# Kernel tuning notes

Hardware: AMD Instinct MI355X
Metric: run time of the kernel (lower is better)

## Reference

```python
import jax, jax.numpy as jnp
import numpy as np

N0 = N1 = N2 = N3 = 8          # input_shape
R = 8                           # input_ranks (rank_i)
L = 8                           # link_ranks (ring bond dims)
OR = 64                         # output_rank
OF = 1024                       # output_features
B = 4096                        # batch
STD = 0.09                      # ~calculate_std() for this config


def setup_inputs() -> dict:
    key = jax.random.key(0)
    ks = jax.random.split(key, 9)
    x = jax.random.normal(ks[0], (B, N0, N1, N2, N3), dtype=jnp.float32)
    # factor_i: (n_i, link_left, link_right, rank_i)
    f0 = jax.random.normal(ks[1], (N0, L, L, R), dtype=jnp.float32) * STD
    f1 = jax.random.normal(ks[2], (N1, L, L, R), dtype=jnp.float32) * STD
    f2 = jax.random.normal(ks[3], (N2, L, L, R), dtype=jnp.float32) * STD
    f3 = jax.random.normal(ks[4], (N3, L, L, R), dtype=jnp.float32) * STD
    core = jax.random.normal(ks[5], (R, R, R, R, OR), dtype=jnp.float32) * STD
    out_factor = jax.random.normal(ks[6], (OR, OF), dtype=jnp.float32) * STD
    bound = 1.0 / np.sqrt(N0 * N1 * N2 * N3)
    bias = jax.random.uniform(ks[7], (OF,), dtype=jnp.float32, minval=-bound, maxval=bound)
    return {"x": x, "f0": f0, "f1": f1, "f2": f2, "f3": f3,
            "core": core, "out_factor": out_factor, "bias": bias}


def _tr_weight(f0, f1, f2, f3, core, out_factor):
    # Contract the tensor-ring (factors + core + output factor) into the
    # effective weight W[n0,n1,n2,n3,out]. Contraction order chosen so every
    # intermediate stays small; result equals tn.contractors.greedy output.
    # core axes: p=r0, q=r1, s=r2, t=r3, o=out_rank; links a,b,c,d close the ring.
    t1 = jnp.einsum('iabp,pqsto->iabqsto', f0, core)      # [n0,L,L,r1,r2,r3,or]
    t2 = jnp.einsum('jbcq,iabqsto->ijacsto', f1, t1)      # [n0,n1,L,L,r2,r3,or]
    t3 = jnp.einsum('kcds,ijacsto->ijkadto', f2, t2)      # [n0,n1,n2,L,L,r3,or]
    t4 = jnp.einsum('ldat,ijkadto->ijklo', f3, t3)        # ring trace -> [n0..n3,or]
    return jnp.einsum('ijklo,of->ijklf', t4, out_factor)  # [n0,n1,n2,n3,out]


def reference(x, f0, f1, f2, f3, core, out_factor, bias):
    W = _tr_weight(f0, f1, f2, f3, core, out_factor)      # [8,8,8,8,1024]
    out = jnp.einsum('bijkl,ijklf->bf', x, W)             # [B, out_features]
    return out + bias
```

## Files before the change

### kernel.cpp

```cpp
#include <hip/hip_runtime.h>


#define WS_NEED ((size_t)12386304 * 4)

typedef __attribute__((ext_vector_type(8))) short short8v;
typedef __attribute__((ext_vector_type(4))) float f32x4;

__device__ inline unsigned short f2bf(float f) {
  unsigned u = __builtin_bit_cast(unsigned, f);
  u += 0x7FFFu + ((u >> 16) & 1u);
  return (unsigned short)(u >> 16);
}
__device__ inline float bf2f(unsigned short h) {
  return __builtin_bit_cast(float, (unsigned)h << 16);
}


__global__ __launch_bounds__(256) void k_build(const float* __restrict__ f0,
                                               const float* __restrict__ f1,
                                               const float* __restrict__ f2,
                                               const float* __restrict__ f3,
                                               float* __restrict__ G01,
                                               float* __restrict__ G23) {
  int bb = blockIdx.x, tid = threadIdx.x;
  __shared__ float lu[512], lv[512];
  bool is01 = bb < 64;
  int pairi = is01 ? bb : bb - 64;
  int iA = pairi >> 3, iB = pairi & 7;
  const float* fu = is01 ? f0 : f2;
  const float* fv = is01 ? f1 : f3;
  if (tid < 128)
    reinterpret_cast<float4*>(lu)[tid] = reinterpret_cast<const float4*>(fu + iA * 512)[tid];
  else
    reinterpret_cast<float4*>(lv)[tid - 128] = reinterpret_cast<const float4*>(fv + iB * 512)[tid - 128];
  __syncthreads();
  float* dst = is01 ? G01 : G23;
#pragma unroll
  for (int r = 0; r < 16; ++r) {
    int idx = r * 256 + tid;
    int uv = idx >> 6, pq = idx & 63;
    int a = uv >> 3, c = uv & 7, p = pq >> 3, q = pq & 7;
    float acc = 0.f;
    if (is01) {
#pragma unroll
      for (int b = 0; b < 8; ++b)
        acc = fmaf(lu[a * 64 + b * 8 + p], lv[b * 64 + c * 8 + q], acc);
    } else {
#pragma unroll
      for (int d = 0; d < 8; ++d)
        acc = fmaf(lu[c * 64 + d * 8 + p], lv[d * 64 + a * 8 + q], acc);
    }
    dst[pairi * 4096 + idx] = acc;
  }
}


__global__ __launch_bounds__(256) void k_packs(const float* __restrict__ G01,
                                               const float* __restrict__ G23,
                                               const float* __restrict__ core,
                                               unsigned short* __restrict__ G01p,
                                               unsigned short* __restrict__ CP,
                                               unsigned short* __restrict__ G23p) {
  int bb = blockIdx.x, tid = threadIdx.x;
  __shared__ float ls[4096];
  if (bb < 64) {
    int ij = bb;
#pragma unroll
    for (int r = 0; r < 4; ++r)
      reinterpret_cast<float4*>(ls)[r * 256 + tid] =
          reinterpret_cast<const float4*>(G01 + ij * 4096)[r * 256 + tid];
    __syncthreads();
    short8v* dst = reinterpret_cast<short8v*>(G01p);
#pragma unroll
    for (int it = 0; it < 2; ++it) {
      int item = it * 256 + tid;
      int ks = item >> 8, mf = (item >> 6) & 3, l = item & 63;
      short8v hi, lo;
#pragma unroll
      for (int j = 0; j < 8; ++j) {
        float v = ls[(mf * 16 + (l & 15)) * 64 + ks * 32 + 8 * (l >> 4) + j];
        unsigned short h = f2bf(v);
        hi[j] = (short)h; lo[j] = (short)f2bf(v - bf2f(h));
      }
      size_t base = ((((size_t)ij * 2 + ks) * 4 + mf) * 2) * 64 + l;
      dst[base] = hi; dst[base + 64] = lo;
    }
  } else if (bb < 128) {
    int st = bb - 64;
#pragma unroll
    for (int r = 0; r < 4; ++r) {
      int f4 = r * 256 + tid;
      reinterpret_cast<float4*>(ls)[f4] =
          reinterpret_cast<const float4*>(core)[(f4 >> 4) * 1024 + st * 16 + (f4 & 15)];
    }
    __syncthreads();
    short8v* dst = reinterpret_cast<short8v*>(CP);
#pragma unroll
    for (int it = 0; it < 2; ++it) {
      int item = it * 256 + tid;
      int ks = item >> 8, nf = (item >> 6) & 3, l = item & 63;
      short8v hi, lo;
#pragma unroll
      for (int j = 0; j < 8; ++j) {
        float v = ls[(ks * 32 + 8 * (l >> 4) + j) * 64 + nf * 16 + (l & 15)];
        unsigned short h = f2bf(v);
        hi[j] = (short)h; lo[j] = (short)f2bf(v - bf2f(h));
      }
      size_t base = ((((size_t)st * 2 + ks) * 4 + nf) * 2) * 64 + l;
      dst[base] = hi; dst[base + 64] = lo;
    }
  } else {
    int ks = bb - 128;
    int st = ks >> 1, acb = (ks & 1) * 32;
#pragma unroll
    for (int r = 0; r < 8; ++r) {
      int idx = r * 256 + tid;
      ls[idx] = G23[(idx >> 5) * 4096 + (acb + (idx & 31)) * 64 + st];
    }
    __syncthreads();
    short8v* dst = reinterpret_cast<short8v*>(G23p);
    int mf = tid >> 6, l = tid & 63;
    short8v hi, lo;
#pragma unroll
    for (int j = 0; j < 8; ++j) {
      float v = ls[(mf * 16 + (l & 15)) * 32 + 8 * (l >> 4) + j];
      unsigned short h = f2bf(v);
      hi[j] = (short)h; lo[j] = (short)f2bf(v - bf2f(h));
    }
    size_t base = (((size_t)ks * 4 + mf) * 2) * 64 + l;
    dst[base] = hi; dst[base + 64] = lo;
  }
}


__global__ __launch_bounds__(256) void k_dmat(const unsigned short* __restrict__ G01p,
                                              const unsigned short* __restrict__ CP,
                                              unsigned short* __restrict__ Dp,
                                              int h) {
  int bid = blockIdx.x;
  int ij = bid >> 6, st = bid & 63;
  int w = threadIdx.x >> 6, l = threadIdx.x & 63;
  const short8v* gp = reinterpret_cast<const short8v*>(G01p);
  const short8v* cp = reinterpret_cast<const short8v*>(CP);
  short8v ah0 = gp[((((size_t)ij * 2 + 0) * 4 + w) * 2) * 64 + l];
  short8v al0 = gp[((((size_t)ij * 2 + 0) * 4 + w) * 2) * 64 + 64 + l];
  short8v ah1 = gp[((((size_t)ij * 2 + 1) * 4 + w) * 2) * 64 + l];
  short8v al1 = gp[((((size_t)ij * 2 + 1) * 4 + w) * 2) * 64 + 64 + l];
  f32x4 acc[2];
  acc[0] = (f32x4){0.f, 0.f, 0.f, 0.f};
  acc[1] = acc[0];
#pragma unroll
  for (int n2 = 0; n2 < 2; ++n2) {
    int nf = 2 * h + n2;
    short8v bh0 = cp[((((size_t)st * 2 + 0) * 4 + nf) * 2) * 64 + l];
    short8v bl0 = cp[((((size_t)st * 2 + 0) * 4 + nf) * 2) * 64 + 64 + l];
    short8v bh1 = cp[((((size_t)st * 2 + 1) * 4 + nf) * 2) * 64 + l];
    short8v bl1 = cp[((((size_t)st * 2 + 1) * 4 + nf) * 2) * 64 + 64 + l];
    acc[n2] = __builtin_amdgcn_mfma_f32_16x16x32_bf16(ah0, bh0, acc[n2], 0, 0, 0);
    acc[n2] = __builtin_amdgcn_mfma_f32_16x16x32_bf16(al0, bh0, acc[n2], 0, 0, 0);
    acc[n2] = __builtin_amdgcn_mfma_f32_16x16x32_bf16(ah0, bl0, acc[n2], 0, 0, 0);
    acc[n2] = __builtin_amdgcn_mfma_f32_16x16x32_bf16(ah1, bh1, acc[n2], 0, 0, 0);
    acc[n2] = __builtin_amdgcn_mfma_f32_16x16x32_bf16(al1, bh1, acc[n2], 0, 0, 0);
    acc[n2] = __builtin_amdgcn_mfma_f32_16x16x32_bf16(ah1, bl1, acc[n2], 0, 0, 0);
  }
  __shared__ float lds[64 * 34];
#pragma unroll
  for (int n2 = 0; n2 < 2; ++n2)
#pragma unroll
    for (int r = 0; r < 4; ++r)
      lds[(w * 16 + 4 * (l >> 4) + r) * 34 + n2 * 16 + (l & 15)] = acc[n2][r];
  __syncthreads();
  int t = threadIdx.x;
  int a2 = t >> 7, n2p = (t >> 6) & 1, l2 = t & 63;
  short8v hi, lo;
#pragma unroll
  for (int j = 0; j < 8; ++j) {
    float v = lds[(a2 * 32 + 8 * (l2 >> 4) + j) * 34 + n2p * 16 + (l2 & 15)];
    unsigned short hh = f2bf(v);
    hi[j] = (short)hh; lo[j] = (short)f2bf(v - bf2f(hh));
  }
  short8v* dst = reinterpret_cast<short8v*>(Dp);
  size_t base = ((((size_t)ij * 128 + st * 2 + a2) * 2 + n2p) * 2) * 64 + l2;
  dst[base] = hi; dst[base + 64] = lo;
}


__global__ __launch_bounds__(256) void k_t4mm(const unsigned short* __restrict__ G23p,
                                              const unsigned short* __restrict__ Dp,
                                              float* __restrict__ T4part,
                                              int h) {
  int bid = blockIdx.x;
  int ij = bid >> 3, kc = bid & 7;
  int w = threadIdx.x >> 6, l = threadIdx.x & 63;
  const short8v* ga = reinterpret_cast<const short8v*>(G23p);
  const short8v* gb = reinterpret_cast<const short8v*>(Dp);
  f32x4 acc0 = {0.f, 0.f, 0.f, 0.f}, acc1 = acc0;
#pragma unroll 2
  for (int ks = kc * 16; ks < kc * 16 + 16; ++ks) {
    size_t abase = (((size_t)ks * 4 + w) * 2) * 64 + l;
    short8v ah = ga[abase], al = ga[abase + 64];
    size_t bbase = (((size_t)ij * 128 + ks) * 4) * 64 + l;
    short8v bh0 = gb[bbase],       bl0 = gb[bbase + 64];
    short8v bh1 = gb[bbase + 128], bl1 = gb[bbase + 192];
    acc0 = __builtin_amdgcn_mfma_f32_16x16x32_bf16(ah, bh0, acc0, 0, 0, 0);
    acc0 = __builtin_amdgcn_mfma_f32_16x16x32_bf16(al, bh0, acc0, 0, 0, 0);
    acc0 = __builtin_amdgcn_mfma_f32_16x16x32_bf16(ah, bl0, acc0, 0, 0, 0);
    acc1 = __builtin_amdgcn_mfma_f32_16x16x32_bf16(ah, bh1, acc1, 0, 0, 0);
    acc1 = __builtin_amdgcn_mfma_f32_16x16x32_bf16(al, bh1, acc1, 0, 0, 0);
    acc1 = __builtin_amdgcn_mfma_f32_16x16x32_bf16(ah, bl1, acc1, 0, 0, 0);
  }
#pragma unroll
  for (int r = 0; r < 4; ++r) {
    int row = w * 16 + 4 * (l >> 4) + r;
    T4part[(((size_t)kc * 64 + ij) * 64 + row) * 64 + h * 32 + (l & 15)] = acc0[r];
    T4part[(((size_t)kc * 64 + ij) * 64 + row) * 64 + h * 32 + 16 + (l & 15)] = acc1[r];
  }
}


__global__ __launch_bounds__(256) void k_pack2(const float* __restrict__ T4part,
                                               unsigned short* __restrict__ Bp) {
  int kb = blockIdx.x, tid = threadIdx.x;
  __shared__ float ls[2048];
  f32x4 a0 = {0.f, 0.f, 0.f, 0.f}, a1 = a0;
#pragma unroll
  for (int kc = 0; kc < 8; ++kc) {
    const f32x4* src = reinterpret_cast<const f32x4*>(T4part + (size_t)kc * 262144 + kb * 2048);
    a0 += src[tid];
    a1 += src[256 + tid];
  }
  reinterpret_cast<f32x4*>(ls)[tid] = a0;
  reinterpret_cast<f32x4*>(ls)[256 + tid] = a1;
  __syncthreads();
  short8v* dst = reinterpret_cast<short8v*>(Bp);
  int nf = tid >> 6, l = tid & 63;
  short8v hi, lo;
#pragma unroll
  for (int j = 0; j < 8; ++j) {
    float v = ls[(8 * (l >> 4) + j) * 64 + nf * 16 + (l & 15)];
    unsigned short h = f2bf(v);
    hi[j] = (short)h; lo[j] = (short)f2bf(v - bf2f(h));
  }
  size_t base = (size_t)kb * 512 + (nf * 2) * 64 + l;
  dst[base] = hi; dst[base + 64] = lo;
}


__global__ __launch_bounds__(256) void k_ymm(const float* __restrict__ x,
                                             const unsigned short* __restrict__ Bp,
                                             float* __restrict__ Ypart) {
  int mt = blockIdx.x >> 4, kc = blockIdx.x & 15;
  int w = threadIdx.x >> 6, l = threadIdx.x & 63;
  int kg = l >> 4, lm = l & 15;
  const float4* xp = reinterpret_cast<const float4*>(
      x + (size_t)(mt * 64 + w * 16 + lm) * 4096 + kc * 256 + kg * 8);
  f32x4 acc0 = {0.f, 0.f, 0.f, 0.f}, acc1 = acc0, acc2 = acc0, acc3 = acc0;
#pragma unroll 1
  for (int s = 0; s < 8; ++s) {
    float4 xa = xp[s * 8], xb = xp[s * 8 + 1];
    float xs[8] = {xa.x, xa.y, xa.z, xa.w, xb.x, xb.y, xb.z, xb.w};
    short8v ah, al;
#pragma unroll
    for (int j = 0; j < 8; ++j) {
      unsigned short h = f2bf(xs[j]);
      ah[j] = (short)h;
      al[j] = (short)f2bf(xs[j] - bf2f(h));
    }
    const short8v* bp = reinterpret_cast<const short8v*>(Bp + (size_t)(kc * 8 + s) * 4096) + l;
    short8v bh0 = bp[0],   bl0 = bp[64];
    short8v bh1 = bp[128], bl1 = bp[192];
    short8v bh2 = bp[256], bl2 = bp[320];
    short8v bh3 = bp[384], bl3 = bp[448];
    acc0 = __builtin_amdgcn_mfma_f32_16x16x32_bf16(ah, bh0, acc0, 0, 0, 0);
    acc1 = __builtin_amdgcn_mfma_f32_16x16x32_bf16(ah, bh1, acc1, 0, 0, 0);
    acc2 = __builtin_amdgcn_mfma_f32_16x16x32_bf16(ah, bh2, acc2, 0, 0, 0);
    acc3 = __builtin_amdgcn_mfma_f32_16x16x32_bf16(ah, bh3, acc3, 0, 0, 0);
    acc0 = __builtin_amdgcn_mfma_f32_16x16x32_bf16(al, bh0, acc0, 0, 0, 0);
    acc1 = __builtin_amdgcn_mfma_f32_16x16x32_bf16(al, bh1, acc1, 0, 0, 0);
    acc2 = __builtin_amdgcn_mfma_f32_16x16x32_bf16(al, bh2, acc2, 0, 0, 0);
    acc3 = __builtin_amdgcn_mfma_f32_16x16x32_bf16(al, bh3, acc3, 0, 0, 0);
    acc0 = __builtin_amdgcn_mfma_f32_16x16x32_bf16(ah, bl0, acc0, 0, 0, 0);
    acc1 = __builtin_amdgcn_mfma_f32_16x16x32_bf16(ah, bl1, acc1, 0, 0, 0);
    acc2 = __builtin_amdgcn_mfma_f32_16x16x32_bf16(ah, bl2, acc2, 0, 0, 0);
    acc3 = __builtin_amdgcn_mfma_f32_16x16x32_bf16(ah, bl3, acc3, 0, 0, 0);
  }
  float* yb = Ypart + (size_t)kc * 262144 + (size_t)(mt * 64 + w * 16) * 64;
#pragma unroll
  for (int r = 0; r < 4; ++r) {
    yb[(kg * 4 + r) * 64 + 0  + lm] = acc0[r];
    yb[(kg * 4 + r) * 64 + 16 + lm] = acc1[r];
    yb[(kg * 4 + r) * 64 + 32 + lm] = acc2[r];
    yb[(kg * 4 + r) * 64 + 48 + lm] = acc3[r];
  }
}


__global__ __launch_bounds__(256) void k_yred(const float* __restrict__ Ypart,
                                              const float* __restrict__ OF_,
                                              unsigned short* __restrict__ Yp,
                                              unsigned short* __restrict__ OFp) {
  int bb = blockIdx.x, tid = threadIdx.x;
  __shared__ float ls[8192];
  if (bb < 64) {
    f32x4 a[4];
#pragma unroll
    for (int r = 0; r < 4; ++r) a[r] = (f32x4){0.f, 0.f, 0.f, 0.f};
#pragma unroll
    for (int kc = 0; kc < 16; ++kc) {
      const f32x4* src = reinterpret_cast<const f32x4*>(Ypart + (size_t)kc * 262144 + (size_t)bb * 4096);
#pragma unroll
      for (int r = 0; r < 4; ++r) a[r] += src[r * 256 + tid];
    }
#pragma unroll
    for (int r = 0; r < 4; ++r) reinterpret_cast<f32x4*>(ls)[r * 256 + tid] = a[r];
    __syncthreads();
    short8v* dst = reinterpret_cast<short8v*>(Yp);
#pragma unroll
    for (int it = 0; it < 2; ++it) {
      int item = it * 256 + tid;
      int mtl = item >> 7, ks = (item >> 6) & 1, l = item & 63;
      short8v hi, lo;
#pragma unroll
      for (int j = 0; j < 8; ++j) {
        float v = ls[(mtl * 16 + (l & 15)) * 64 + ks * 32 + 8 * (l >> 4) + j];
        unsigned short h = f2bf(v);
        hi[j] = (short)h; lo[j] = (short)f2bf(v - bf2f(h));
      }
      int mtu = bb * 4 + mtl;
      size_t base = (((size_t)mtu * 2 + ks) * 2) * 64 + l;
      dst[base] = hi; dst[base + 64] = lo;
    }
  } else {
    int g = bb - 64;
#pragma unroll
    for (int it = 0; it < 8; ++it) {
      int f4 = it * 256 + tid;
      reinterpret_cast<float4*>(ls)[f4] =
          reinterpret_cast<const float4*>(OF_)[(f4 >> 5) * 256 + g * 32 + (f4 & 31)];
    }
    __syncthreads();
    short8v* dst = reinterpret_cast<short8v*>(OFp);
#pragma unroll
    for (int it = 0; it < 4; ++it) {
      int item = it * 256 + tid;
      int nfl = item >> 7, ks = (item >> 6) & 1, l = item & 63;
      short8v hi, lo;
#pragma unroll
      for (int j = 0; j < 8; ++j) {
        float v = ls[(ks * 32 + 8 * (l >> 4) + j) * 128 + nfl * 16 + (l & 15)];
        unsigned short h = f2bf(v);
        hi[j] = (short)h; lo[j] = (short)f2bf(v - bf2f(h));
      }
      int nfg = g * 8 + nfl;
      size_t base = (((size_t)nfg * 2 + ks) * 2) * 64 + l;
      dst[base] = hi; dst[base + 64] = lo;
    }
  }
}


__global__ __launch_bounds__(256) void k_out3(const unsigned short* __restrict__ Yp,
                                              const unsigned short* __restrict__ OFp,
                                              const float* __restrict__ bias,
                                              float* __restrict__ out) {
  int bid = blockIdx.x;
  int mtile = bid >> 2, nch = bid & 3;
  int w = threadIdx.x >> 6, l = threadIdx.x & 63;
  int mtu = mtile * 4 + w;
  const short8v* yp = reinterpret_cast<const short8v*>(Yp);
  const short8v* op = reinterpret_cast<const short8v*>(OFp);
  short8v ya0 = yp[(((size_t)mtu * 2 + 0) * 2) * 64 + l];
  short8v yl0 = yp[(((size_t)mtu * 2 + 0) * 2) * 64 + 64 + l];
  short8v ya1 = yp[(((size_t)mtu * 2 + 1) * 2) * 64 + l];
  short8v yl1 = yp[(((size_t)mtu * 2 + 1) * 2) * 64 + 64 + l];
#pragma unroll 4
  for (int nf = 0; nf < 16; ++nf) {
    int nfg = nch * 16 + nf;
    size_t bb = (((size_t)nfg * 2) * 2) * 64 + l;
    short8v bh0 = op[bb], bl0 = op[bb + 64], bh1 = op[bb + 128], bl1 = op[bb + 192];
    f32x4 acc = {0.f, 0.f, 0.f, 0.f};
    acc = __builtin_amdgcn_mfma_f32_16x16x32_bf16(ya0, bh0, acc, 0, 0, 0);
    acc = __builtin_amdgcn_mfma_f32_16x16x32_bf16(yl0, bh0, acc, 0, 0, 0);
    acc = __builtin_amdgcn_mfma_f32_16x16x32_bf16(ya0, bl0, acc, 0, 0, 0);
    acc = __builtin_amdgcn_mfma_f32_16x16x32_bf16(ya1, bh1, acc, 0, 0, 0);
    acc = __builtin_amdgcn_mfma_f32_16x16x32_bf16(yl1, bh1, acc, 0, 0, 0);
    acc = __builtin_amdgcn_mfma_f32_16x16x32_bf16(ya1, bl1, acc, 0, 0, 0);
    float bv = bias[nfg * 16 + (l & 15)];
#pragma unroll
    for (int r = 0; r < 4; ++r)
      out[(size_t)(mtile * 64 + w * 16 + 4 * (l >> 4) + r) * 1024 + nfg * 16 + (l & 15)] = acc[r] + bv;
  }
}


__global__ __launch_bounds__(256) void k_t4(const float* __restrict__ A,
                                            const float* __restrict__ B,
                                            const float* __restrict__ core,
                                            float* __restrict__ T4) {
  int bid = blockIdx.x;
  int ij = bid >> 4, kl0 = (bid & 15) * 4;
  __shared__ float lA[4096];
  __shared__ float lS[4][4096];
  int tid = threadIdx.x;
#pragma unroll
  for (int r = 0; r < 4; ++r)
    reinterpret_cast<float4*>(lA)[r * 256 + tid] =
        reinterpret_cast<const float4*>(A + ij * 4096)[r * 256 + tid];
  __syncthreads();
  int pq0 = (tid >> 4) << 2;
  int st04 = tid & 15;
#pragma unroll 1
  for (int m = 0; m < 4; ++m) {
    const float4* Bp = reinterpret_cast<const float4*>(B + (kl0 + m) * 4096);
    float acc[4][4] = {{0.f}};
    for (int ac = 0; ac < 64; ++ac) {
      float4 av = reinterpret_cast<float4*>(lA)[ac * 16 + (pq0 >> 2)];
      float4 bv = Bp[ac * 16 + st04];
      float au[4] = {av.x, av.y, av.z, av.w};
      float bu[4] = {bv.x, bv.y, bv.z, bv.w};
#pragma unroll
      for (int u = 0; u < 4; ++u)
#pragma unroll
        for (int v = 0; v < 4; ++v)
          acc[u][v] = fmaf(au[u], bu[v], acc[u][v]);
    }
    float4* S4 = reinterpret_cast<float4*>(lS[m]);
#pragma unroll
    for (int u = 0; u < 4; ++u)
      S4[(pq0 + u) * 16 + st04] = make_float4(acc[u][0], acc[u][1], acc[u][2], acc[u][3]);
  }
  __syncthreads();
  int o44 = tid & 15, seg = tid >> 4;
  const float4* c4 = reinterpret_cast<const float4*>(core);
  float4 r0 = {0, 0, 0, 0}, r1 = r0, r2 = r0, r3 = r0;
  for (int n = 0; n < 256; ++n) {
    int midx = seg * 256 + n;
    float4 cv = c4[midx * 16 + o44];
    float s0 = lS[0][midx], s1 = lS[1][midx], s2 = lS[2][midx], s3 = lS[3][midx];
    r0.x = fmaf(s0, cv.x, r0.x); r0.y = fmaf(s0, cv.y, r0.y);
    r0.z = fmaf(s0, cv.z, r0.z); r0.w = fmaf(s0, cv.w, r0.w);
    r1.x = fmaf(s1, cv.x, r1.x); r1.y = fmaf(s1, cv.y, r1.y);
    r1.z = fmaf(s1, cv.z, r1.z); r1.w = fmaf(s1, cv.w, r1.w);
    r2.x = fmaf(s2, cv.x, r2.x); r2.y = fmaf(s2, cv.y, r2.y);
    r2.z = fmaf(s2, cv.z, r2.z); r2.w = fmaf(s2, cv.w, r2.w);
    r3.x = fmaf(s3, cv.x, r3.x); r3.y = fmaf(s3, cv.y, r3.y);
    r3.z = fmaf(s3, cv.z, r3.z); r3.w = fmaf(s3, cv.w, r3.w);
  }
  float4* red = reinterpret_cast<float4*>(lA);
  red[(seg * 4 + 0) * 16 + o44] = r0;
  red[(seg * 4 + 1) * 16 + o44] = r1;
  red[(seg * 4 + 2) * 16 + o44] = r2;
  red[(seg * 4 + 3) * 16 + o44] = r3;
  __syncthreads();
  int m2 = tid >> 6, o = tid & 63;
  float t = 0.f;
#pragma unroll
  for (int s2 = 0; s2 < 16; ++s2) t += lA[(s2 * 4 + m2) * 64 + o];
  T4[(ij * 64 + kl0 + m2) * 64 + o] = t;
}

__global__ __launch_bounds__(256) void k_y(const float* __restrict__ x,
                                           const float* __restrict__ T4,
                                           float* __restrict__ Y) {
  int b0 = blockIdx.x * 16;
  __shared__ float lx[1024];
  int tid = threadIdx.x;
  int o = tid & 63, rg = tid >> 6;
  float acc0 = 0.f, acc1 = 0.f, acc2 = 0.f, acc3 = 0.f;
  const float4* lx4 = reinterpret_cast<const float4*>(lx);
  for (int kc = 0; kc < 4096; kc += 64) {
    __syncthreads();
    reinterpret_cast<float4*>(lx)[tid] =
        *reinterpret_cast<const float4*>(x + (b0 + (tid >> 4)) * 4096 + kc + (tid & 15) * 4);
    __syncthreads();
#pragma unroll 4
    for (int kk = 0; kk < 64; kk += 4) {
      float c0 = T4[(kc + kk + 0) * 64 + o];
      float c1 = T4[(kc + kk + 1) * 64 + o];
      float c2 = T4[(kc + kk + 2) * 64 + o];
      float c3 = T4[(kc + kk + 3) * 64 + o];
      float4 xv;
      xv = lx4[(rg * 4 + 0) * 16 + (kk >> 2)];
      acc0 = fmaf(xv.x, c0, fmaf(xv.y, c1, fmaf(xv.z, c2, fmaf(xv.w, c3, acc0))));
      xv = lx4[(rg * 4 + 1) * 16 + (kk >> 2)];
      acc1 = fmaf(xv.x, c0, fmaf(xv.y, c1, fmaf(xv.z, c2, fmaf(xv.w, c3, acc1))));
      xv = lx4[(rg * 4 + 2) * 16 + (kk >> 2)];
      acc2 = fmaf(xv.x, c0, fmaf(xv.y, c1, fmaf(xv.z, c2, fmaf(xv.w, c3, acc2))));
      xv = lx4[(rg * 4 + 3) * 16 + (kk >> 2)];
      acc3 = fmaf(xv.x, c0, fmaf(xv.y, c1, fmaf(xv.z, c2, fmaf(xv.w, c3, acc3))));
    }
  }
  Y[(b0 + rg * 4 + 0) * 64 + o] = acc0;
  Y[(b0 + rg * 4 + 1) * 64 + o] = acc1;
  Y[(b0 + rg * 4 + 2) * 64 + o] = acc2;
  Y[(b0 + rg * 4 + 3) * 64 + o] = acc3;
}

__global__ __launch_bounds__(256) void k_out(const float* __restrict__ Y,
                                             const float* __restrict__ OF_,
                                             const float* __restrict__ bias,
                                             float* __restrict__ out) {
  int b0 = blockIdx.x * 16;
  int tid = threadIdx.x;
  __shared__ float lY[1024];
  reinterpret_cast<float4*>(lY)[tid] =
      *reinterpret_cast<const float4*>(Y + (b0 + (tid >> 4)) * 64 + (tid & 15) * 4);
  __syncthreads();
  float4 acc[16];
#pragma unroll
  for (int r = 0; r < 16; ++r) acc[r] = make_float4(0.f, 0.f, 0.f, 0.f);
  for (int oo = 0; oo < 64; ++oo) {
    float4 w = *reinterpret_cast<const float4*>(OF_ + oo * 1024 + tid * 4);
#pragma unroll
    for (int r = 0; r < 16; ++r) {
      float yv = lY[r * 64 + oo];
      acc[r].x = fmaf(yv, w.x, acc[r].x);
      acc[r].y = fmaf(yv, w.y, acc[r].y);
      acc[r].z = fmaf(yv, w.z, acc[r].z);
      acc[r].w = fmaf(yv, w.w, acc[r].w);
    }
  }
  float4 bv = *reinterpret_cast<const float4*>(bias + tid * 4);
#pragma unroll
  for (int r = 0; r < 16; ++r) {
    float4 v = acc[r];
    v.x += bv.x; v.y += bv.y; v.z += bv.z; v.w += bv.w;
    *reinterpret_cast<float4*>(out + (b0 + r) * 1024 + tid * 4) = v;
  }
}


extern "C" void kernel_launch(void* const* d_in, const int* in_sizes, int n_in,
                              void* d_out, int out_size, void* d_ws, size_t ws_size,
                              hipStream_t stream) {
  const float* x    = (const float*)d_in[0];
  const float* f0   = (const float*)d_in[1];
  const float* f1   = (const float*)d_in[2];
  const float* f2   = (const float*)d_in[3];
  const float* f3   = (const float*)d_in[4];
  const float* core = (const float*)d_in[5];
  const float* ofac = (const float*)d_in[6];
  const float* bias = (const float*)d_in[7];
  float* out = (float*)d_out;
  float* ws = (float*)d_ws;

  float* G01 = ws;
  float* G23 = ws + 262144;

  k_build<<<128, 256, 0, stream>>>(f0, f1, f2, f3, G01, G23);

  if (ws_size >= WS_NEED) {
    unsigned short* G01p = (unsigned short*)(ws + 524288);
    unsigned short* CP   = (unsigned short*)(ws + 786432);
    unsigned short* G23p = (unsigned short*)(ws + 1048576);
    unsigned short* Bp   = (unsigned short*)(ws + 1310720);
    unsigned short* Yp   = (unsigned short*)(ws + 1572864);
    unsigned short* OFp  = (unsigned short*)(ws + 1835008);
    float* T4part = ws + 1900544;
    unsigned short* Dp = (unsigned short*)(ws + 3997696);
    float* Ypart = ws + 3997696;

    k_packs<<<256, 256, 0, stream>>>(G01, G23, core, G01p, CP, G23p);
    for (int h = 0; h < 2; ++h) {
      k_dmat<<<4096, 256, 0, stream>>>(G01p, CP, Dp, h);
      k_t4mm<<<512, 256, 0, stream>>>(G23p, Dp, T4part, h);
    }
    k_pack2<<<128, 256, 0, stream>>>(T4part, Bp);
    k_ymm<<<1024, 256, 0, stream>>>(x, Bp, Ypart);
    k_yred<<<72, 256, 0, stream>>>(Ypart, ofac, Yp, OFp);
    k_out3<<<256, 256, 0, stream>>>(Yp, OFp, bias, out);
  } else {
    float* T4 = ws + 524288;
    float* Yb = ws + 786432;
    k_t4<<<1024, 256, 0, stream>>>(G01, G23, core, T4);
    k_y<<<256, 256, 0, stream>>>(x, T4, Yb);
    k_out<<<256, 256, 0, stream>>>(Yb, ofac, bias, out);
  }
}
```

Baseline: 188.2 us.

## Merge half passes, fold output-factor packing and Y reduction into fewer kernels

Removes the two-pass loop over output halves so the D-matrix build and T4 matmul each run once over all four column fragments, which needs a larger workspace for Dp. Output-factor packing moves into the initial pack kernel, and the Y partial-sum reduction is fused into the final output GEMM, dropping the separate yred kernel. The x split into bf16 hi/lo now truncates instead of rounding. Together these cut the launch count from nine to six and drop intermediate round-trips, at the cost of more registers per thread and a larger workspace requirement.

```diff
diff --git a/kernel.cpp b/kernel.cpp
--- a/kernel.cpp
+++ b/kernel.cpp
@@ -1,7 +1,7 @@
 #include <hip/hip_runtime.h>
 
 
-#define WS_NEED ((size_t)12386304 * 4)
+#define WS_NEED ((size_t)25231360 * 4)
 
 typedef __attribute__((ext_vector_type(8))) short short8v;
 typedef __attribute__((ext_vector_type(4))) float f32x4;
@@ -58,11 +58,13 @@
 __global__ __launch_bounds__(256) void k_packs(const float* __restrict__ G01,
                                                const float* __restrict__ G23,
                                                const float* __restrict__ core,
+                                               const float* __restrict__ OF_,
                                                unsigned short* __restrict__ G01p,
                                                unsigned short* __restrict__ CP,
-                                               unsigned short* __restrict__ G23p) {
+                                               unsigned short* __restrict__ G23p,
+                                               unsigned short* __restrict__ OFp) {
   int bb = blockIdx.x, tid = threadIdx.x;
-  __shared__ float ls[4096];
+  __shared__ float ls[8192];
   if (bb < 64) {
     int ij = bb;
 #pragma unroll
@@ -109,7 +111,7 @@
       size_t base = ((((size_t)st * 2 + ks) * 4 + nf) * 2) * 64 + l;
       dst[base] = hi; dst[base + 64] = lo;
     }
-  } else {
+  } else if (bb < 256) {
     int ks = bb - 128;
     int st = ks >> 1, acb = (ks & 1) * 32;
 #pragma unroll
@@ -129,14 +131,38 @@
     }
     size_t base = (((size_t)ks * 4 + mf) * 2) * 64 + l;
     dst[base] = hi; dst[base + 64] = lo;
+  } else {
+    int g = bb - 256;
+#pragma unroll
+    for (int it = 0; it < 8; ++it) {
+      int f4 = it * 256 + tid;
+      reinterpret_cast<float4*>(ls)[f4] =
+          reinterpret_cast<const float4*>(OF_)[(f4 >> 5) * 256 + g * 32 + (f4 & 31)];
+    }
+    __syncthreads();
+    short8v* dst = reinterpret_cast<short8v*>(OFp);
+#pragma unroll
+    for (int it = 0; it < 4; ++it) {
+      int item = it * 256 + tid;
+      int nfl = item >> 7, ks = (item >> 6) & 1, l = item & 63;
+      short8v hi, lo;
+#pragma unroll
+      for (int j = 0; j < 8; ++j) {
+        float v = ls[(ks * 32 + 8 * (l >> 4) + j) * 128 + nfl * 16 + (l & 15)];
+        unsigned short h = f2bf(v);
+        hi[j] = (short)h; lo[j] = (short)f2bf(v - bf2f(h));
+      }
+      int nfg = g * 8 + nfl;
+      size_t base = (((size_t)nfg * 2 + ks) * 2) * 64 + l;
+      dst[base] = hi; dst[base + 64] = lo;
+    }
   }
 }
 
 
 __global__ __launch_bounds__(256) void k_dmat(const unsigned short* __restrict__ G01p,
                                               const unsigned short* __restrict__ CP,
-                                              unsigned short* __restrict__ Dp,
-                                              int h) {
+                                              unsigned short* __restrict__ Dp) {
   int bid = blockIdx.x;
   int ij = bid >> 6, st = bid & 63;
   int w = threadIdx.x >> 6, l = threadIdx.x & 63;
@@ -146,75 +172,79 @@
   short8v al0 = gp[((((size_t)ij * 2 + 0) * 4 + w) * 2) * 64 + 64 + l];
   short8v ah1 = gp[((((size_t)ij * 2 + 1) * 4 + w) * 2) * 64 + l];
   short8v al1 = gp[((((size_t)ij * 2 + 1) * 4 + w) * 2) * 64 + 64 + l];
-  f32x4 acc[2];
-  acc[0] = (f32x4){0.f, 0.f, 0.f, 0.f};
-  acc[1] = acc[0];
-#pragma unroll
-  for (int n2 = 0; n2 < 2; ++n2) {
-    int nf = 2 * h + n2;
+  f32x4 acc[4];
+#pragma unroll
+  for (int nf = 0; nf < 4; ++nf) acc[nf] = (f32x4){0.f, 0.f, 0.f, 0.f};
+#pragma unroll
+  for (int nf = 0; nf < 4; ++nf) {
     short8v bh0 = cp[((((size_t)st * 2 + 0) * 4 + nf) * 2) * 64 + l];
     short8v bl0 = cp[((((size_t)st * 2 + 0) * 4 + nf) * 2) * 64 + 64 + l];
     short8v bh1 = cp[((((size_t)st * 2 + 1) * 4 + nf) * 2) * 64 + l];
     short8v bl1 = cp[((((size_t)st * 2 + 1) * 4 + nf) * 2) * 64 + 64 + l];
-    acc[n2] = __builtin_amdgcn_mfma_f32_16x16x32_bf16(ah0, bh0, acc[n2], 0, 0, 0);
-    acc[n2] = __builtin_amdgcn_mfma_f32_16x16x32_bf16(al0, bh0, acc[n2], 0, 0, 0);
-    acc[n2] = __builtin_amdgcn_mfma_f32_16x16x32_bf16(ah0, bl0, acc[n2], 0, 0, 0);
-    acc[n2] = __builtin_amdgcn_mfma_f32_16x16x32_bf16(ah1, bh1, acc[n2], 0, 0, 0);
-    acc[n2] = __builtin_amdgcn_mfma_f32_16x16x32_bf16(al1, bh1, acc[n2], 0, 0, 0);
-    acc[n2] = __builtin_amdgcn_mfma_f32_16x16x32_bf16(ah1, bl1, acc[n2], 0, 0, 0);
-  }
-  __shared__ float lds[64 * 34];
-#pragma unroll
-  for (int n2 = 0; n2 < 2; ++n2)
+    acc[nf] = __builtin_amdgcn_mfma_f32_16x16x32_bf16(ah0, bh0, acc[nf], 0, 0, 0);
+    acc[nf] = __builtin_amdgcn_mfma_f32_16x16x32_bf16(al0, bh0, acc[nf], 0, 0, 0);
+    acc[nf] = __builtin_amdgcn_mfma_f32_16x16x32_bf16(ah0, bl0, acc[nf], 0, 0, 0);
+    acc[nf] = __builtin_amdgcn_mfma_f32_16x16x32_bf16(ah1, bh1, acc[nf], 0, 0, 0);
+    acc[nf] = __builtin_amdgcn_mfma_f32_16x16x32_bf16(al1, bh1, acc[nf], 0, 0, 0);
+    acc[nf] = __builtin_amdgcn_mfma_f32_16x16x32_bf16(ah1, bl1, acc[nf], 0, 0, 0);
+  }
+  __shared__ float lds[64 * 66];
+#pragma unroll
+  for (int nf = 0; nf < 4; ++nf)
 #pragma unroll
     for (int r = 0; r < 4; ++r)
-      lds[(w * 16 + 4 * (l >> 4) + r) * 34 + n2 * 16 + (l & 15)] = acc[n2][r];
-  __syncthreads();
-  int t = threadIdx.x;
-  int a2 = t >> 7, n2p = (t >> 6) & 1, l2 = t & 63;
-  short8v hi, lo;
-#pragma unroll
-  for (int j = 0; j < 8; ++j) {
-    float v = lds[(a2 * 32 + 8 * (l2 >> 4) + j) * 34 + n2p * 16 + (l2 & 15)];
-    unsigned short hh = f2bf(v);
-    hi[j] = (short)hh; lo[j] = (short)f2bf(v - bf2f(hh));
-  }
+      lds[(w * 16 + 4 * (l >> 4) + r) * 66 + nf * 16 + (l & 15)] = acc[nf][r];
+  __syncthreads();
   short8v* dst = reinterpret_cast<short8v*>(Dp);
-  size_t base = ((((size_t)ij * 128 + st * 2 + a2) * 2 + n2p) * 2) * 64 + l2;
-  dst[base] = hi; dst[base + 64] = lo;
+#pragma unroll
+  for (int it = 0; it < 2; ++it) {
+    int item = it * 256 + threadIdx.x;
+    int a2 = item >> 8, nf = (item >> 6) & 3, l2 = item & 63;
+    short8v hi, lo;
+#pragma unroll
+    for (int j = 0; j < 8; ++j) {
+      float v = lds[(a2 * 32 + 8 * (l2 >> 4) + j) * 66 + nf * 16 + (l2 & 15)];
+      unsigned short hh = f2bf(v);
+      hi[j] = (short)hh; lo[j] = (short)f2bf(v - bf2f(hh));
+    }
+    int ks = st * 2 + a2;
+    size_t base = ((((size_t)ij * 128 + ks) * 4 + nf) * 2) * 64 + l2;
+    dst[base] = hi; dst[base + 64] = lo;
+  }
 }
 
 
 __global__ __launch_bounds__(256) void k_t4mm(const unsigned short* __restrict__ G23p,
                                               const unsigned short* __restrict__ Dp,
-                                              float* __restrict__ T4part,
-                                              int h) {
+                                              float* __restrict__ T4part) {
   int bid = blockIdx.x;
   int ij = bid >> 3, kc = bid & 7;
   int w = threadIdx.x >> 6, l = threadIdx.x & 63;
   const short8v* ga = reinterpret_cast<const short8v*>(G23p);
   const short8v* gb = reinterpret_cast<const short8v*>(Dp);
-  f32x4 acc0 = {0.f, 0.f, 0.f, 0.f}, acc1 = acc0;
+  f32x4 acc[4];
+#pragma unroll
+  for (int nf = 0; nf < 4; ++nf) acc[nf] = (f32x4){0.f, 0.f, 0.f, 0.f};
 #pragma unroll 2
   for (int ks = kc * 16; ks < kc * 16 + 16; ++ks) {
     size_t abase = (((size_t)ks * 4 + w) * 2) * 64 + l;
     short8v ah = ga[abase], al = ga[abase + 64];
-    size_t bbase = (((size_t)ij * 128 + ks) * 4) * 64 + l;
-    short8v bh0 = gb[bbase],       bl0 = gb[bbase + 64];
-    short8v bh1 = gb[bbase + 128], bl1 = gb[bbase + 192];
-    acc0 = __builtin_amdgcn_mfma_f32_16x16x32_bf16(ah, bh0, acc0, 0, 0, 0);
-    acc0 = __builtin_amdgcn_mfma_f32_16x16x32_bf16(al, bh0, acc0, 0, 0, 0);
-    acc0 = __builtin_amdgcn_mfma_f32_16x16x32_bf16(ah, bl0, acc0, 0, 0, 0);
-    acc1 = __builtin_amdgcn_mfma_f32_16x16x32_bf16(ah, bh1, acc1, 0, 0, 0);
-    acc1 = __builtin_amdgcn_mfma_f32_16x16x32_bf16(al, bh1, acc1, 0, 0, 0);
-    acc1 = __builtin_amdgcn_mfma_f32_16x16x32_bf16(ah, bl1, acc1, 0, 0, 0);
-  }
-#pragma unroll
-  for (int r = 0; r < 4; ++r) {
-    int row = w * 16 + 4 * (l >> 4) + r;
-    T4part[(((size_t)kc * 64 + ij) * 64 + row) * 64 + h * 32 + (l & 15)] = acc0[r];
-    T4part[(((size_t)kc * 64 + ij) * 64 + row) * 64 + h * 32 + 16 + (l & 15)] = acc1[r];
-  }
+#pragma unroll
+    for (int nf = 0; nf < 4; ++nf) {
+      size_t bbase = ((((size_t)ij * 128 + ks) * 4 + nf) * 2) * 64 + l;
+      short8v bh = gb[bbase], bl = gb[bbase + 64];
+      acc[nf] = __builtin_amdgcn_mfma_f32_16x16x32_bf16(ah, bh, acc[nf], 0, 0, 0);
+      acc[nf] = __builtin_amdgcn_mfma_f32_16x16x32_bf16(al, bh, acc[nf], 0, 0, 0);
+      acc[nf] = __builtin_amdgcn_mfma_f32_16x16x32_bf16(ah, bl, acc[nf], 0, 0, 0);
+    }
+  }
+#pragma unroll
+  for (int nf = 0; nf < 4; ++nf)
+#pragma unroll
+    for (int r = 0; r < 4; ++r) {
+      int row = w * 16 + 4 * (l >> 4) + r;
+      T4part[(((size_t)kc * 64 + ij) * 64 + row) * 64 + nf * 16 + (l & 15)] = acc[nf][r];
+    }
 }
 
 
@@ -262,9 +292,11 @@
     short8v ah, al;
 #pragma unroll
     for (int j = 0; j < 8; ++j) {
-      unsigned short h = f2bf(xs[j]);
+      unsigned u = __builtin_bit_cast(unsigned, xs[j]);
+      unsigned short h = (unsigned short)(u >> 16);
       ah[j] = (short)h;
-      al[j] = (short)f2bf(xs[j] - bf2f(h));
+      float lo = xs[j] - bf2f(h);
+      al[j] = (short)(__builtin_bit_cast(unsigned, lo) >> 16);
     }
     const short8v* bp = reinterpret_cast<const short8v*>(Bp + (size_t)(kc * 8 + s) * 4096) + l;
     short8v bh0 = bp[0],   bl0 = bp[64];
@@ -295,87 +327,36 @@
 }
 
 
-__global__ __launch_bounds__(256) void k_yred(const float* __restrict__ Ypart,
-                                              const float* __restrict__ OF_,
-                                              unsigned short* __restrict__ Yp,
-                                              unsigned short* __restrict__ OFp) {
-  int bb = blockIdx.x, tid = threadIdx.x;
-  __shared__ float ls[8192];
-  if (bb < 64) {
-    f32x4 a[4];
-#pragma unroll
-    for (int r = 0; r < 4; ++r) a[r] = (f32x4){0.f, 0.f, 0.f, 0.f};
-#pragma unroll
-    for (int kc = 0; kc < 16; ++kc) {
-      const f32x4* src = reinterpret_cast<const f32x4*>(Ypart + (size_t)kc * 262144 + (size_t)bb * 4096);
-#pragma unroll
-      for (int r = 0; r < 4; ++r) a[r] += src[r * 256 + tid];
-    }
-#pragma unroll
-    for (int r = 0; r < 4; ++r) reinterpret_cast<f32x4*>(ls)[r * 256 + tid] = a[r];
-    __syncthreads();
-    short8v* dst = reinterpret_cast<short8v*>(Yp);
-#pragma unroll
-    for (int it = 0; it < 2; ++it) {
-      int item = it * 256 + tid;
-      int mtl = item >> 7, ks = (item >> 6) & 1, l = item & 63;
-      short8v hi, lo;
-#pragma unroll
-      for (int j = 0; j < 8; ++j) {
-        float v = ls[(mtl * 16 + (l & 15)) * 64 + ks * 32 + 8 * (l >> 4) + j];
-        unsigned short h = f2bf(v);
-        hi[j] = (short)h; lo[j] = (short)f2bf(v - bf2f(h));
-      }
-      int mtu = bb * 4 + mtl;
-      size_t base = (((size_t)mtu * 2 + ks) * 2) * 64 + l;
-      dst[base] = hi; dst[base + 64] = lo;
-    }
-  } else {
-    int g = bb - 64;
-#pragma unroll
-    for (int it = 0; it < 8; ++it) {
-      int f4 = it * 256 + tid;
-      reinterpret_cast<float4*>(ls)[f4] =
-          reinterpret_cast<const float4*>(OF_)[(f4 >> 5) * 256 + g * 32 + (f4 & 31)];
-    }
-    __syncthreads();
-    short8v* dst = reinterpret_cast<short8v*>(OFp);
-#pragma unroll
-    for (int it = 0; it < 4; ++it) {
-      int item = it * 256 + tid;
-      int nfl = item >> 7, ks = (item >> 6) & 1, l = item & 63;
-      short8v hi, lo;
-#pragma unroll
-      for (int j = 0; j < 8; ++j) {
-        float v = ls[(ks * 32 + 8 * (l >> 4) + j) * 128 + nfl * 16 + (l & 15)];
-        unsigned short h = f2bf(v);
-        hi[j] = (short)h; lo[j] = (short)f2bf(v - bf2f(h));
-      }
-      int nfg = g * 8 + nfl;
-      size_t base = (((size_t)nfg * 2 + ks) * 2) * 64 + l;
-      dst[base] = hi; dst[base + 64] = lo;
-    }
-  }
-}
-
-
-__global__ __launch_bounds__(256) void k_out3(const unsigned short* __restrict__ Yp,
+__global__ __launch_bounds__(256) void k_out4(const float* __restrict__ Ypart,
                                               const unsigned short* __restrict__ OFp,
                                               const float* __restrict__ bias,
                                               float* __restrict__ out) {
-  int bid = blockIdx.x;
-  int mtile = bid >> 2, nch = bid & 3;
-  int w = threadIdx.x >> 6, l = threadIdx.x & 63;
-  int mtu = mtile * 4 + w;
-  const short8v* yp = reinterpret_cast<const short8v*>(Yp);
+  int mt16 = blockIdx.x;
+  int tid = threadIdx.x;
+  __shared__ float ls[1024];
+  {
+    f32x4 a = {0.f, 0.f, 0.f, 0.f};
+#pragma unroll
+    for (int kc = 0; kc < 16; ++kc)
+      a += *reinterpret_cast<const f32x4*>(Ypart + (size_t)kc * 262144 + (size_t)mt16 * 1024 + tid * 4);
+    *reinterpret_cast<f32x4*>(ls + tid * 4) = a;
+  }
+  __syncthreads();
+  int w = tid >> 6, l = tid & 63;
+  short8v ya0, yl0, ya1, yl1;
+#pragma unroll
+  for (int j = 0; j < 8; ++j) {
+    float v0 = ls[(l & 15) * 64 + 0  + 8 * (l >> 4) + j];
+    float v1 = ls[(l & 15) * 64 + 32 + 8 * (l >> 4) + j];
+    unsigned short h0 = (unsigned short)(__builtin_bit_cast(unsigned, v0) >> 16);
+    unsigned short h1 = (unsigned short)(__builtin_bit_cast(unsigned, v1) >> 16);
+    ya0[j] = (short)h0; yl0[j] = (short)(__builtin_bit_cast(unsigned, v0 - bf2f(h0)) >> 16);
+    ya1[j] = (short)h1; yl1[j] = (short)(__builtin_bit_cast(unsigned, v1 - bf2f(h1)) >> 16);
+  }
   const short8v* op = reinterpret_cast<const short8v*>(OFp);
-  short8v ya0 = yp[(((size_t)mtu * 2 + 0) * 2) * 64 + l];
-  short8v yl0 = yp[(((size_t)mtu * 2 + 0) * 2) * 64 + 64 + l];
-  short8v ya1 = yp[(((size_t)mtu * 2 + 1) * 2) * 64 + l];
-  short8v yl1 = yp[(((size_t)mtu * 2 + 1) * 2) * 64 + 64 + l];
 #pragma unroll 4
   for (int nf = 0; nf < 16; ++nf) {
-    int nfg = nch * 16 + nf;
+    int nfg = w * 16 + nf;
     size_t bb = (((size_t)nfg * 2) * 2) * 64 + l;
     short8v bh0 = op[bb], bl0 = op[bb + 64], bh1 = op[bb + 128], bl1 = op[bb + 192];
     f32x4 acc = {0.f, 0.f, 0.f, 0.f};
@@ -388,7 +369,7 @@
     float bv = bias[nfg * 16 + (l & 15)];
 #pragma unroll
     for (int r = 0; r < 4; ++r)
-      out[(size_t)(mtile * 64 + w * 16 + 4 * (l >> 4) + r) * 1024 + nfg * 16 + (l & 15)] = acc[r] + bv;
+      out[(size_t)(mt16 * 16 + 4 * (l >> 4) + r) * 1024 + nfg * 16 + (l & 15)] = acc[r] + bv;
   }
 }
 
@@ -552,23 +533,19 @@
   if (ws_size >= WS_NEED) {
     unsigned short* G01p = (unsigned short*)(ws + 524288);
     unsigned short* CP   = (unsigned short*)(ws + 786432);
-    unsigned short* G23p = (unsigned short*)(ws + 1048576);
-    unsigned short* Bp   = (unsigned short*)(ws + 1310720);
-    unsigned short* Yp   = (unsigned short*)(ws + 1572864);
-    unsigned short* OFp  = (unsigned short*)(ws + 1835008);
-    float* T4part = ws + 1900544;
-    unsigned short* Dp = (unsigned short*)(ws + 3997696);
-    float* Ypart = ws + 3997696;
-
-    k_packs<<<256, 256, 0, stream>>>(G01, G23, core, G01p, CP, G23p);
-    for (int h = 0; h < 2; ++h) {
-      k_dmat<<<4096, 256, 0, stream>>>(G01p, CP, Dp, h);
-      k_t4mm<<<512, 256, 0, stream>>>(G23p, Dp, T4part, h);
-    }
+    unsigned short* G23p = (unsigned short*)(ws + 1310720);
+    unsigned short* Bp   = (unsigned short*)(ws + 1835008);
+    unsigned short* OFp  = (unsigned short*)(ws + 2097152);
+    float* T4part = ws + 2162688;
+    float* Ypart  = ws + 4259840;
+    unsigned short* Dp = (unsigned short*)(ws + 8454144);
+
+    k_packs<<<264, 256, 0, stream>>>(G01, G23, core, ofac, G01p, CP, G23p, OFp);
+    k_dmat<<<4096, 256, 0, stream>>>(G01p, CP, Dp);
+    k_t4mm<<<512, 256, 0, stream>>>(G23p, Dp, T4part);
     k_pack2<<<128, 256, 0, stream>>>(T4part, Bp);
     k_ymm<<<1024, 256, 0, stream>>>(x, Bp, Ypart);
-    k_yred<<<72, 256, 0, stream>>>(Ypart, ofac, Yp, OFp);
-    k_out3<<<256, 256, 0, stream>>>(Yp, OFp, bias, out);
+    k_out4<<<256, 256, 0, stream>>>(Ypart, OFp, bias, out);
   } else {
     float* T4 = ws + 524288;
     float* Yb = ws + 786432;
```

Measured after the change: 178.7 us. 5.0% less time.
